# Kernel optimization log

Measured on AMD Instinct MI355X. Metric: run time of the kernel, lower is better.

Reference implementation:

```python
import jax, jax.numpy as jnp
import numpy as np
import math

INF = 1e12  # constant.INFINITY_NUMBER in the original repo


def setup_inputs() -> dict:
    key = jax.random.key(0)
    ks = jax.random.split(key, 12)
    B, S, W, D = 16, 512, 8, 768
    M, Wm = 2, 64
    U, Wu = 32, 16
    V = 32000
    words = jax.random.randint(ks[0], (B, S, W), 0, V)
    masks = jax.random.randint(ks[1], (B, S, W), 0, 2).astype(bool)
    main = jax.random.randint(ks[2], (B, M, Wm), 0, V)
    main_mask = jax.random.randint(ks[3], (B, M, Wm), 0, 2).astype(bool)
    user = jax.random.randint(ks[4], (B, U, Wu), 0, V)
    user_mask = jax.random.randint(ks[5], (B, U, Wu), 0, 2).astype(bool)
    # sparse-ish dependency adjacency
    adj = (jax.random.uniform(ks[6], (B, S, S)) < 0.05).astype(jnp.float32)
    emb_weight = jax.random.normal(ks[7], (V, D), jnp.float32) * 0.02
    K_w = jax.random.normal(ks[8], (D, D), jnp.float32) * (1.0 / math.sqrt(D))
    K_b = jnp.zeros((D,), jnp.float32)
    Q_w = jax.random.normal(ks[9], (D, D), jnp.float32) * (1.0 / math.sqrt(D))
    Q_b = jnp.zeros((D,), jnp.float32)
    return {"words": words, "masks": masks, "main": main, "main_mask": main_mask,
            "user": user, "user_mask": user_mask, "adj": adj,
            "emb_weight": emb_weight, "K_w": K_w, "K_b": K_b, "Q_w": Q_w, "Q_b": Q_b}


def _masked_max(embs, mask, axis):
    # masked_fill(mask, -INF) -> max(axis) ; caller fixes residual -INF rows
    return jnp.max(jnp.where(mask[..., None], -INF, embs), axis=axis)


def reference(words, masks, main, main_mask, user, user_mask, adj,
              emb_weight, K_w, K_b, Q_w, Q_b):
    D = emb_weight.shape[1]

    word_embs = emb_weight[words]   # [B,S,W,D]
    main_embs = emb_weight[main]    # [B,M,Wm,D]
    user_embs = emb_weight[user]    # [B,U,Wu,D]

    # node mask from adjacency: True where node has no in/out edges
    mask = ((adj.sum(axis=2) + adj.sum(axis=1)) == 0)[:, :, None]  # [B,S,1]

    # main: masked max-pool over word pieces, zero fully-masked rows
    main_e = _masked_max(main_embs, main_mask, axis=2)             # [B,M,D]
    main_e = jnp.where(main_e == -INF, 0.0, main_e)

    # user: masked max-pool over word pieces then over users
    user_e = _masked_max(user_embs, user_mask, axis=2)             # [B,U,D]
    user_e = jnp.max(user_e, axis=1)                               # [B,D]
    user_e = jnp.where(user_e == -INF, 0.0, user_e)

    # token embeddings: masked max-pool over word pieces (no -INF fix in original)
    g = _masked_max(word_embs, masks, axis=2)                      # [B,S,D]

    # single-head attention: softmax(K g (Q g)^T / sqrt(D)) @ g
    key_ = g @ K_w.T + K_b                                         # [B,S,D]
    query = g @ Q_w.T + Q_b                                        # [B,S,D]
    scores = jnp.einsum('bsd,btd->bst', key_, query) / math.sqrt(D)
    dense_graph = jax.nn.softmax(scores, axis=2)                   # [B,S,S]
    gcn_out = jnp.einsum('bst,btd->bsd', dense_graph, g)           # [B,S,D]

    adj_sm = jax.nn.softmax(adj, axis=2)

    return (gcn_out, mask, dense_graph, adj_sm,
            jnp.squeeze(main_e), jnp.squeeze(user_e))
```

## Files before the change

### kernel.cpp

```cpp
#include <hip/hip_runtime.h>
#include <hip/hip_bf16.h>
#include <math.h>

static constexpr int Bn = 16, Sn = 512, Wn = 8, Dn = 768;
static constexpr int Mn_ = 2, WMn = 64;
static constexpr int Un = 32, WUn = 16;

#define INF_VAL 1e12f
#define INV_SQRT_D 0.03608439182435161f

static constexpr size_t OFF_GCN   = 0;
static constexpr size_t OFF_MASK  = 6291456;
static constexpr size_t OFF_DENSE = 6299648;
static constexpr size_t OFF_ADJ   = 10493952;
static constexpr size_t OFF_MAIN  = 14688256;
static constexpr size_t OFF_USER  = 14712832;

static constexpr size_t WSB_GBF     = 0;
static constexpr size_t WSB_GT      = 12582912;
static constexpr size_t WSB_DENSEBF = 25165824;
static constexpr size_t WSB_HBF     = 33554432;
static constexpr size_t WSB_KWT     = 46137344;
static constexpr size_t WSB_QWT     = 47316992;
static constexpr size_t WSB_MT      = 48496640;
static constexpr size_t WSB_PARTU   = 49676288;
static constexpr size_t WSB_PARTM   = 51249152;
static constexpr size_t WSB_KBAR    = 51642368;
static constexpr size_t WSB_QBAR    = 51648512;
static constexpr size_t WSB_U       = 51654656;
static constexpr size_t WSB_V       = 51660800;
static constexpr size_t WSB_VA      = 51666944;
static constexpr size_t WSB_VB      = 51673088;
static constexpr size_t WSB_CONSTS  = 51679232;
static constexpr size_t WSB_QS      = 51679296;
static constexpr size_t WSB_KQ      = 51712064;
static constexpr size_t WSB_GA      = 51744832;
static constexpr size_t WSB_GB      = 51777600;
static constexpr size_t WSB_COLSUM  = 51810368;
static constexpr size_t WSB_FLAGS   = 51843136;
static constexpr size_t WSB_ROWSUM  = 51875904;
static constexpr size_t WSB_UVU     = 51908672;
static constexpr size_t WSB_UVV     = 51957824;
static constexpr size_t WSB_UVA     = 52006976;
static constexpr size_t WSB_UVB     = 52056128;

typedef __attribute__((ext_vector_type(8))) short short8;
typedef __attribute__((ext_vector_type(4))) float f32x4;

static __device__ __forceinline__ ushort f2bf(float f) {
    union { float f; unsigned u; } v; v.f = f;
    unsigned u = v.u;
    unsigned r = (u + 0x7FFFu + ((u >> 16) & 1u)) >> 16;
    return (ushort)r;
}

static __device__ __forceinline__ void gload16(const void* g, void* lds) {
    __builtin_amdgcn_global_load_lds(
        (const __attribute__((address_space(1))) void*)g,
        (__attribute__((address_space(3))) void*)lds, 16, 0, 0);
}

static __device__ __forceinline__ void fmax4(float4& a, const float4& x) {
    a.x = fmaxf(a.x, x.x); a.y = fmaxf(a.y, x.y);
    a.z = fmaxf(a.z, x.z); a.w = fmaxf(a.w, x.w);
}

__global__ __launch_bounds__(256)
void fold1(const float* __restrict__ K_w, const float* __restrict__ K_b,
           const float* __restrict__ Q_w, const float* __restrict__ Q_b,
           double* __restrict__ kbar, double* __restrict__ qbar,
           ushort* __restrict__ KwbT, ushort* __restrict__ QwbT,
           float* __restrict__ colsum) {
    int blk = blockIdx.x, t = threadIdx.x;
    if (blk < 192) {
        int wv = t >> 6, lane = t & 63;
        int r = blk * 4 + wv;
        double sk = 0.0, sq = 0.0;
        for (int d = lane; d < Dn; d += 64) {
            sk += (double)K_w[(size_t)r * Dn + d];
            sq += (double)Q_w[(size_t)r * Dn + d];
        }
        #pragma unroll
        for (int off = 32; off > 0; off >>= 1) {
            sk += __shfl_down(sk, off, 64);
            sq += __shfl_down(sq, off, 64);
        }
        if (lane == 0) {
            kbar[r] = -1e12 * sk + (double)K_b[r];
            qbar[r] = -1e12 * sq + (double)Q_b[r];
        }
    } else if (blk < 1344) {
        int tt = blk - 192;
        const float* src = (tt < 576) ? K_w : Q_w;
        ushort* dst = (tt < 576) ? KwbT : QwbT;
        int t6 = (tt < 576) ? tt : tt - 576;
        int e0 = (t6 % 24) * 32, i0 = (t6 / 24) * 32;
        __shared__ ushort tile[32][33];
        int tx = t & 31, ty = t >> 5;
        #pragma unroll
        for (int i2 = 0; i2 < 4; ++i2)
            tile[ty + i2 * 8][tx] = f2bf(src[(size_t)(e0 + ty + i2 * 8) * Dn + i0 + tx]);
        __syncthreads();
        #pragma unroll
        for (int i2 = 0; i2 < 4; ++i2)
            dst[(size_t)(i0 + ty + i2 * 8) * Dn + e0 + tx] = tile[tx][ty + i2 * 8];
    } else {
        for (int i = t; i < Bn * Sn; i += 256) colsum[i] = 0.f;
    }
}

__global__ __launch_bounds__(512)
void adjsm_uv_kernel(const float* __restrict__ adj, float* __restrict__ adjsm,
                     float* __restrict__ colsum, float* __restrict__ rowsum,
                     const float* __restrict__ K_w, const float* __restrict__ Q_w,
                     const float* __restrict__ K_b, const float* __restrict__ Q_b,
                     const double* __restrict__ kbar, const double* __restrict__ qbar,
                     double* __restrict__ uvu, double* __restrict__ uvv,
                     double* __restrict__ uva, double* __restrict__ uvb) {
    int blk = blockIdx.x;
    int t = threadIdx.x;
    if (blk >= 512) {
        int id = (blk - 512) * 512 + t;
        int c = id / 768;
        int j = id - c * 768;
        int e0 = c * 96;
        double su = 0.0, sv = 0.0, sa = 0.0, sb = 0.0;
        for (int e = e0; e < e0 + 96; ++e) {
            double kw = (double)K_w[(size_t)e * Dn + j];
            double qw = (double)Q_w[(size_t)e * Dn + j];
            su += kw * qbar[e];
            sv += qw * kbar[e];
            sa += kw * (double)Q_b[e];
            sb += qw * (double)K_b[e];
        }
        uvu[(size_t)c * Dn + j] = su;
        uvv[(size_t)c * Dn + j] = sv;
        uva[(size_t)c * Dn + j] = sa;
        uvb[(size_t)c * Dn + j] = sb;
        return;
    }
    int b = blk >> 5, rc = blk & 31;
    const float* base = adj + ((size_t)b * Sn + rc * 16) * Sn;
    float* obase = adjsm + ((size_t)b * Sn + rc * 16) * Sn;
    const float EM1 = 0.36787944117144233f;
    const float EP1 = 2.718281828459045f;
    __shared__ float red[8];
    float colacc = 0.f;
    for (int r = 0; r < 16; ++r) {
        float a = base[(size_t)r * Sn + t];
        colacc += a;
        float s = a;
        #pragma unroll
        for (int off = 32; off > 0; off >>= 1) s += __shfl_down(s, off, 64);
        if ((t & 63) == 0) red[t >> 6] = s;
        __syncthreads();
        float n1 = red[0] + red[1] + red[2] + red[3]
                 + red[4] + red[5] + red[6] + red[7];
        float e1, e0;
        if (n1 > 0.f) { e1 = 1.f; e0 = EM1; } else { e1 = EP1; e0 = 1.f; }
        float denom = n1 * e1 + (512.f - n1) * e0;
        float inv = 1.f / denom;
        obase[(size_t)r * Sn + t] = (a == 1.f ? e1 : e0) * inv;
        if (t == 0) rowsum[(size_t)b * Sn + rc * 16 + r] = n1;
        __syncthreads();
    }
    atomicAdd(&colsum[(size_t)b * Sn + t], colacc);
}

__global__ __launch_bounds__(64)
void uvred_consts(const double* __restrict__ uvu, const double* __restrict__ uvv,
                  const double* __restrict__ uva, const double* __restrict__ uvb,
                  const double* __restrict__ kbar, const double* __restrict__ qbar,
                  const float* __restrict__ K_b, const float* __restrict__ Q_b,
                  double* __restrict__ u, double* __restrict__ v,
                  double* __restrict__ va, double* __restrict__ vb,
                  double* __restrict__ consts) {
    int blk = blockIdx.x;
    int l = threadIdx.x;
    if (blk < 12) {
        int j = blk * 64 + l;
        double su = 0.0, sv = 0.0, sa = 0.0, sb = 0.0;
        #pragma unroll
        for (int c = 0; c < 8; ++c) {
            su += uvu[(size_t)c * Dn + j];
            sv += uvv[(size_t)c * Dn + j];
            sa += uva[(size_t)c * Dn + j];
            sb += uvb[(size_t)c * Dn + j];
        }
        u[j] = su; v[j] = sv; va[j] = sa; vb[j] = sb;
    } else {
        double c0 = 0.0, c1 = 0.0, c2 = 0.0, c3 = 0.0;
        for (int e = l; e < Dn; e += 64) {
            c0 += kbar[e] * (double)Q_b[e];
            c1 += kbar[e] * qbar[e];
            c2 += qbar[e] * (double)K_b[e];
            c3 += (double)K_b[e] * (double)Q_b[e];
        }
        #pragma unroll
        for (int off = 32; off > 0; off >>= 1) {
            c0 += __shfl_down(c0, off, 64);
            c1 += __shfl_down(c1, off, 64);
            c2 += __shfl_down(c2, off, 64);
            c3 += __shfl_down(c3, off, 64);
        }
        if (l == 0) { consts[0] = c0; consts[1] = c1; consts[2] = c2; consts[3] = c3; }
    }
}

__global__ __launch_bounds__(192)
void pool_g_s1(const int* __restrict__ words, const int* __restrict__ masks,
               const int* __restrict__ main_idx, const int* __restrict__ mmask,
               const int* __restrict__ user_idx, const int* __restrict__ umask,
               const float* __restrict__ emb,
               const double* __restrict__ u, const double* __restrict__ v,
               const double* __restrict__ va, const double* __restrict__ vb,
               const double* __restrict__ consts,
               ushort* __restrict__ gbf, float* __restrict__ qs,
               float* __restrict__ kq, float* __restrict__ ga,
               float* __restrict__ gb, int* __restrict__ flags,
               float* __restrict__ partM, float* __restrict__ partU) {
    int blk = blockIdx.x;
    int t = threadIdx.x;
    if (blk >= Bn * Sn) {
        int s1 = blk - Bn * Sn;
        const int *irow, *mrow;
        float* dst;
        if (s1 < 128) {
            int bm = s1 >> 2, ch = s1 & 3;
            irow = main_idx + (size_t)bm * WMn + ch * 16;
            mrow = mmask + (size_t)bm * WMn + ch * 16;
            dst = partM + (size_t)s1 * Dn;
        } else {
            int bu = s1 - 128;
            irow = user_idx + (size_t)bu * WUn;
            mrow = umask + (size_t)bu * WUn;
            dst = partU + (size_t)bu * Dn;
        }
        float4 acc = make_float4(-INF_VAL, -INF_VAL, -INF_VAL, -INF_VAL);
        #pragma unroll
        for (int w = 0; w < 16; ++w) {
            if (mrow[w] != 0) continue;
            float4 x = ((const float4*)(emb + (size_t)irow[w] * Dn))[t];
            fmax4(acc, x);
        }
        ((float4*)dst)[t] = acc;
        return;
    }
    int bs = blk;
    const int* wrow = words + (size_t)bs * Wn;
    const int* mrow = masks + (size_t)bs * Wn;
    float4 acc = make_float4(-INF_VAL, -INF_VAL, -INF_VAL, -INF_VAL);
    int nm = 0;
    #pragma unroll
    for (int w = 0; w < Wn; ++w) {
        int mk = mrow[w];
        nm += (mk != 0);
        if (mk != 0) continue;
        float4 x = ((const float4*)(emb + (size_t)wrow[w] * Dn))[t];
        fmax4(acc, x);
    }
    ushort4 o;
    o.x = f2bf(acc.x); o.y = f2bf(acc.y); o.z = f2bf(acc.z); o.w = f2bf(acc.w);
    ((ushort4*)(gbf + (size_t)bs * Dn))[t] = o;
    int j = t * 4;
    double dv = v[j] * (double)acc.x + v[j+1] * (double)acc.y
              + v[j+2] * (double)acc.z + v[j+3] * (double)acc.w;
    double du = u[j] * (double)acc.x + u[j+1] * (double)acc.y
              + u[j+2] * (double)acc.z + u[j+3] * (double)acc.w;
    double da = va[j] * (double)acc.x + va[j+1] * (double)acc.y
              + va[j+2] * (double)acc.z + va[j+3] * (double)acc.w;
    double db = vb[j] * (double)acc.x + vb[j+1] * (double)acc.y
              + vb[j+2] * (double)acc.z + vb[j+3] * (double)acc.w;
    #pragma unroll
    for (int off = 32; off > 0; off >>= 1) {
        dv += __shfl_down(dv, off, 64);
        du += __shfl_down(du, off, 64);
        da += __shfl_down(da, off, 64);
        db += __shfl_down(db, off, 64);
    }
    __shared__ double rr[12];
    if ((t & 63) == 0) {
        rr[t >> 6] = dv; rr[3 + (t >> 6)] = du;
        rr[6 + (t >> 6)] = da; rr[9 + (t >> 6)] = db;
    }
    __syncthreads();
    if (t == 0) {
        qs[bs] = (float)(rr[0] + rr[1] + rr[2] + consts[0]);
        kq[bs] = (float)(rr[3] + rr[4] + rr[5] + consts[2]);
        ga[bs] = (float)(rr[6] + rr[7] + rr[8]);
        gb[bs] = (float)(rr[9] + rr[10] + rr[11]);
        flags[bs] = (nm == Wn) ? 1 : 0;
    }
}

__global__ __launch_bounds__(256)
void mid_kernel(const ushort* __restrict__ gbf, ushort* __restrict__ gT,
                const float* __restrict__ partM, const float* __restrict__ partU,
                float* __restrict__ outM, float* __restrict__ outU,
                const float* __restrict__ rowsum, const float* __restrict__ colsum,
                float* __restrict__ maskout) {
    int blk = blockIdx.x;
    int t = threadIdx.x;
    if (blk < 6144) {
        __shared__ ushort tile[32][33];
        int b = blk / 384;
        int rem = blk - b * 384;
        int d0 = (rem % 24) * 32, s0 = (rem / 24) * 32;
        int tx = t & 31, ty = t >> 5;
        #pragma unroll
        for (int i = 0; i < 4; ++i)
            tile[ty + i * 8][tx] = gbf[((size_t)(b * Sn + s0 + ty + i * 8)) * Dn + d0 + tx];
        __syncthreads();
        #pragma unroll
        for (int i = 0; i < 4; ++i)
            gT[((size_t)(b * Dn + d0 + ty + i * 8)) * Sn + s0 + tx] = tile[tx][ty + i * 8];
        return;
    }
    if (blk >= 6192) {
        int i = (blk - 6192) * 256 + t;
        if (i < Bn * Sn)
            maskout[i] = ((rowsum[i] + colsum[i]) == 0.f) ? 1.f : 0.f;
        return;
    }
    if (t >= 192) return;
    float4 acc = make_float4(-INF_VAL, -INF_VAL, -INF_VAL, -INF_VAL);
    float* dst;
    if (blk < 6176) {
        int bm = blk - 6144;
        #pragma unroll
        for (int c = 0; c < 4; ++c) {
            float4 x = ((const float4*)(partM + (size_t)(bm * 4 + c) * Dn))[t];
            fmax4(acc, x);
        }
        dst = outM + (size_t)bm * Dn;
    } else {
        int b = blk - 6176;
        for (int u2 = 0; u2 < Un; ++u2) {
            float4 x = ((const float4*)(partU + (size_t)(b * Un + u2) * Dn))[t];
            fmax4(acc, x);
        }
        dst = outU + (size_t)b * Dn;
    }
    if (acc.x == -INF_VAL) acc.x = 0.f;
    if (acc.y == -INF_VAL) acc.y = 0.f;
    if (acc.z == -INF_VAL) acc.z = 0.f;
    if (acc.w == -INF_VAL) acc.w = 0.f;
    ((float4*)dst)[t] = acc;
}

template<int OUT_BF16>
__global__ __launch_bounds__(256)
void gemm_mfma(const ushort* __restrict__ A, const ushort* __restrict__ B,
               void* __restrict__ Cout,
               int Km, int lda, int ldb, int ldc,
               long long sA, long long sB, long long sC) {
    __shared__ ushort As[128 * 128];
    __shared__ ushort Bs[64 * 128];
    const ushort* Ab = A + (size_t)blockIdx.z * sA;
    const ushort* Bb = B + (size_t)blockIdx.z * sB;
    int i0 = blockIdx.y * 128, j0 = blockIdx.x * 64;
    int tid = threadIdx.x;
    int lane = tid & 63, wv = tid >> 6;
    int wr = wv >> 1, wc = wv & 1;
    int ln15 = lane & 15, lkg = lane >> 4;
    int r4 = lane >> 4;
    int c16 = lane & 15;

    f32x4 acc[4][2] = {};

    for (int k0 = 0; k0 < Km; k0 += 128) {
        #pragma unroll
        for (int it = 0; it < 8; ++it) {
            int r = it * 16 + wv * 4 + r4;
            int cc = c16 ^ (r & 15);
            ushort* dstA = As + (it * 4096 + wv * 1024) / 2;
            gload16(Ab + (size_t)(i0 + r) * lda + k0 + cc * 8, dstA);
        }
        #pragma unroll
        for (int it = 0; it < 4; ++it) {
            int r = it * 16 + wv * 4 + r4;
            int cc = c16 ^ (r & 15);
            ushort* dstB = Bs + (it * 4096 + wv * 1024) / 2;
            gload16(Bb + (size_t)(j0 + r) * ldb + k0 + cc * 8, dstB);
        }
        __syncthreads();
        #pragma unroll
        for (int kh = 0; kh < 4; ++kh) {
            short8 af[4], bfr[2];
            int kc = kh * 4 + lkg;
            #pragma unroll
            for (int f = 0; f < 4; ++f) {
                int ra = wr * 64 + f * 16 + ln15;
                af[f] = *(const short8*)((const char*)As + ra * 256 + ((kc ^ (ra & 15)) << 4));
            }
            #pragma unroll
            for (int f = 0; f < 2; ++f) {
                int rb = wc * 32 + f * 16 + ln15;
                bfr[f] = *(const short8*)((const char*)Bs + rb * 256 + ((kc ^ (rb & 15)) << 4));
            }
            #pragma unroll
            for (int fa = 0; fa < 4; ++fa)
                #pragma unroll
                for (int fb = 0; fb < 2; ++fb)
                    acc[fa][fb] = __builtin_amdgcn_mfma_f32_16x16x32_bf16(
                        af[fa], bfr[fb], acc[fa][fb], 0, 0, 0);
        }
        __syncthreads();
    }

    #pragma unroll
    for (int fa = 0; fa < 4; ++fa) {
        #pragma unroll
        for (int fb = 0; fb < 2; ++fb) {
            int n = j0 + wc * 32 + fb * 16 + ln15;
            #pragma unroll
            for (int rr = 0; rr < 4; ++rr) {
                int m = i0 + wr * 64 + fa * 16 + lkg * 4 + rr;
                float val = acc[fa][fb][rr];
                if (OUT_BF16) {
                    ((ushort*)Cout)[(size_t)blockIdx.z * sC + (size_t)m * ldc + n] = f2bf(val);
                } else {
                    ((float*)Cout)[(size_t)blockIdx.z * sC + (size_t)m * ldc + n] = val;
                }
            }
        }
    }
}

__global__ __launch_bounds__(256)
void softmax_fix(float* __restrict__ dense, const int* __restrict__ flags,
                 const float* __restrict__ qs, const float* __restrict__ kq,
                 const float* __restrict__ ga, const float* __restrict__ gb,
                 const double* __restrict__ consts, ushort* __restrict__ densebf) {
    int bs = blockIdx.x;
    int b = bs >> 9;
    int t = threadIdx.x;
    float* row = dense + (size_t)bs * 512;
    int f0 = flags[(b << 9) + t];
    int f1 = flags[(b << 9) + t + 256];
    bool sm = flags[bs] != 0;
    float x0, x1;
    if (sm) {
        float c1i = (float)consts[1] * INV_SQRT_D;
        x0 = f0 ? c1i : qs[(b << 9) + t] * INV_SQRT_D;
        x1 = f1 ? c1i : qs[(b << 9) + t + 256] * INV_SQRT_D;
    } else {
        float kqi = kq[bs] * INV_SQRT_D;
        float corr = ga[bs] + (float)consts[3];
        x0 = f0 ? kqi : (row[t] + corr + gb[(b << 9) + t]) * INV_SQRT_D;
        x1 = f1 ? kqi : (row[t + 256] + corr + gb[(b << 9) + t + 256]) * INV_SQRT_D;
    }
    float m = fmaxf(x0, x1);
    #pragma unroll
    for (int off = 32; off > 0; off >>= 1) m = fmaxf(m, __shfl_down(m, off, 64));
    __shared__ float red[4];
    __shared__ float bmax, bsum;
    if ((t & 63) == 0) red[t >> 6] = m;
    __syncthreads();
    if (t == 0) bmax = fmaxf(fmaxf(red[0], red[1]), fmaxf(red[2], red[3]));
    __syncthreads();
    float mx = bmax;
    float e0 = expf(x0 - mx), e1 = expf(x1 - mx);
    float s = e0 + e1;
    #pragma unroll
    for (int off = 32; off > 0; off >>= 1) s += __shfl_down(s, off, 64);
    if ((t & 63) == 0) red[t >> 6] = s;
    __syncthreads();
    if (t == 0) bsum = red[0] + red[1] + red[2] + red[3];
    __syncthreads();
    float inv = 1.f / bsum;
    float p0 = e0 * inv, p1 = e1 * inv;
    row[t] = p0; row[t + 256] = p1;
    ushort* bro = densebf + (size_t)bs * 512;
    bro[t] = f2bf(p0); bro[t + 256] = f2bf(p1);
}

extern "C" void kernel_launch(void* const* d_in, const int* in_sizes, int n_in,
                              void* d_out, int out_size, void* d_ws, size_t ws_size,
                              hipStream_t stream) {
    const int*   words     = (const int*)d_in[0];
    const int*   masks     = (const int*)d_in[1];
    const int*   main_idx  = (const int*)d_in[2];
    const int*   main_mask = (const int*)d_in[3];
    const int*   user_idx  = (const int*)d_in[4];
    const int*   user_mask = (const int*)d_in[5];
    const float* adj       = (const float*)d_in[6];
    const float* emb       = (const float*)d_in[7];
    const float* K_w       = (const float*)d_in[8];
    const float* K_b       = (const float*)d_in[9];
    const float* Q_w       = (const float*)d_in[10];
    const float* Q_b       = (const float*)d_in[11];

    float* out = (float*)d_out;
    char*  ws8 = (char*)d_ws;

    ushort* gbf     = (ushort*)(ws8 + WSB_GBF);
    ushort* gT      = (ushort*)(ws8 + WSB_GT);
    ushort* densebf = (ushort*)(ws8 + WSB_DENSEBF);
    ushort* hbf     = (ushort*)(ws8 + WSB_HBF);
    ushort* KwbT    = (ushort*)(ws8 + WSB_KWT);
    ushort* QwbT    = (ushort*)(ws8 + WSB_QWT);
    ushort* Mt      = (ushort*)(ws8 + WSB_MT);
    float*  partU   = (float*)(ws8 + WSB_PARTU);
    float*  partM   = (float*)(ws8 + WSB_PARTM);
    double* kbar    = (double*)(ws8 + WSB_KBAR);
    double* qbar    = (double*)(ws8 + WSB_QBAR);
    double* u       = (double*)(ws8 + WSB_U);
    double* v       = (double*)(ws8 + WSB_V);
    double* va      = (double*)(ws8 + WSB_VA);
    double* vb      = (double*)(ws8 + WSB_VB);
    double* consts  = (double*)(ws8 + WSB_CONSTS);
    float*  qs      = (float*)(ws8 + WSB_QS);
    float*  kq      = (float*)(ws8 + WSB_KQ);
    float*  ga      = (float*)(ws8 + WSB_GA);
    float*  gb      = (float*)(ws8 + WSB_GB);
    float*  colsum  = (float*)(ws8 + WSB_COLSUM);
    int*    flags   = (int*)(ws8 + WSB_FLAGS);
    float*  rowsum  = (float*)(ws8 + WSB_ROWSUM);
    double* uvu     = (double*)(ws8 + WSB_UVU);
    double* uvv     = (double*)(ws8 + WSB_UVV);
    double* uva     = (double*)(ws8 + WSB_UVA);
    double* uvb     = (double*)(ws8 + WSB_UVB);

    float* dense = out + OFF_DENSE;

    fold1<<<1345, 256, 0, stream>>>(K_w, K_b, Q_w, Q_b, kbar, qbar, KwbT, QwbT, colsum);

    adjsm_uv_kernel<<<524, 512, 0, stream>>>(adj, out + OFF_ADJ, colsum, rowsum,
                                             K_w, Q_w, K_b, Q_b, kbar, qbar,
                                             uvu, uvv, uva, uvb);

    uvred_consts<<<13, 64, 0, stream>>>(uvu, uvv, uva, uvb, kbar, qbar, K_b, Q_b,
                                        u, v, va, vb, consts);

    gemm_mfma<1><<<dim3(12, 6, 1), 256, 0, stream>>>(
        QwbT, KwbT, Mt, Dn, Dn, Dn, Dn, 0, 0, 0);

    pool_g_s1<<<Bn * Sn + 640, 192, 0, stream>>>(
        words, masks, main_idx, main_mask, user_idx, user_mask, emb,
        u, v, va, vb, consts, gbf, qs, kq, ga, gb, flags, partM, partU);

    mid_kernel<<<6224, 256, 0, stream>>>(gbf, gT, partM, partU,
                                         out + OFF_MAIN, out + OFF_USER,
                                         rowsum, colsum, out + OFF_MASK);

    gemm_mfma<1><<<dim3(12, 64, 1), 256, 0, stream>>>(
        gbf, Mt, hbf, Dn, Dn, Dn, Dn, 0, 0, 0);

    gemm_mfma<0><<<dim3(8, 4, Bn), 256, 0, stream>>>(
        hbf, gbf, dense, Dn, Dn, Dn, Sn,
        (long long)Sn * Dn, (long long)Sn * Dn, (long long)Sn * Sn);

    softmax_fix<<<Bn * Sn, 256, 0, stream>>>(dense, flags, qs, kq, ga, gb, consts, densebf);

    gemm_mfma<0><<<dim3(12, 4, Bn), 256, 0, stream>>>(
        densebf, gT, out + OFF_GCN, Sn, Sn, Sn, Dn,
        (long long)Sn * Sn, (long long)Dn * Sn, (long long)Sn * Dn);
}
```

Measured before the change: 157.3 us.

## Fuse small GEMMs into neighbouring kernels and restructure adjacency softmax row sums

Moves the GEMM body into a device function so it can share a launch with the uv reduction/constants kernel and with the transpose/pool/mask kernel, removing two kernel launches. The adjacency softmax now stages 16 rows in shared memory and computes each row sum once per wave instead of doing a block-wide reduction with syncthreads per row. In exchange, the fused kernels reserve GEMM-sized shared memory for every block, including the many tiny transpose blocks, which can reduce occupancy.

```diff
diff --git a/kernel.cpp b/kernel.cpp
--- a/kernel.cpp
+++ b/kernel.cpp
@@ -144,41 +144,151 @@
     float* obase = adjsm + ((size_t)b * Sn + rc * 16) * Sn;
     const float EM1 = 0.36787944117144233f;
     const float EP1 = 2.718281828459045f;
-    __shared__ float red[8];
+    __shared__ float rows[16][512];
+    __shared__ float n1s[16];
+    #pragma unroll
+    for (int r = 0; r < 16; ++r) rows[r][t] = base[(size_t)r * Sn + t];
+    __syncthreads();
+    int wv = t >> 6, lane = t & 63;
+    #pragma unroll
+    for (int rr2 = 0; rr2 < 2; ++rr2) {
+        int r = wv * 2 + rr2;
+        float s = 0.f;
+        #pragma unroll
+        for (int c = 0; c < 8; ++c) s += rows[r][lane + c * 64];
+        #pragma unroll
+        for (int off = 32; off > 0; off >>= 1) s += __shfl_down(s, off, 64);
+        if (lane == 0) {
+            n1s[r] = s;
+            rowsum[(size_t)b * Sn + rc * 16 + r] = s;
+        }
+    }
+    __syncthreads();
     float colacc = 0.f;
+    #pragma unroll
     for (int r = 0; r < 16; ++r) {
-        float a = base[(size_t)r * Sn + t];
+        float a = rows[r][t];
         colacc += a;
-        float s = a;
-        #pragma unroll
-        for (int off = 32; off > 0; off >>= 1) s += __shfl_down(s, off, 64);
-        if ((t & 63) == 0) red[t >> 6] = s;
-        __syncthreads();
-        float n1 = red[0] + red[1] + red[2] + red[3]
-                 + red[4] + red[5] + red[6] + red[7];
+        float n1 = n1s[r];
         float e1, e0;
         if (n1 > 0.f) { e1 = 1.f; e0 = EM1; } else { e1 = EP1; e0 = 1.f; }
-        float denom = n1 * e1 + (512.f - n1) * e0;
-        float inv = 1.f / denom;
+        float inv = 1.f / (n1 * e1 + (512.f - n1) * e0);
         obase[(size_t)r * Sn + t] = (a == 1.f ? e1 : e0) * inv;
-        if (t == 0) rowsum[(size_t)b * Sn + rc * 16 + r] = n1;
+    }
+    atomicAdd(&colsum[(size_t)b * Sn + t], colacc);
+}
+
+template<int OUT_BF16>
+static __device__ __forceinline__
+void gemm_device(const ushort* __restrict__ A, const ushort* __restrict__ B,
+                 void* __restrict__ Cout, int bx, int by, int bz,
+                 int Km, int lda, int ldb, int ldc,
+                 long long sA, long long sB, long long sC,
+                 ushort* As, ushort* Bs) {
+    const ushort* Ab = A + (size_t)bz * sA;
+    const ushort* Bb = B + (size_t)bz * sB;
+    int i0 = by * 128, j0 = bx * 64;
+    int tid = threadIdx.x;
+    int lane = tid & 63, wv = tid >> 6;
+    int wr = wv >> 1, wc = wv & 1;
+    int ln15 = lane & 15, lkg = lane >> 4;
+    int r4 = lane >> 4;
+    int c16 = lane & 15;
+
+    f32x4 acc[4][2] = {};
+
+    for (int k0 = 0; k0 < Km; k0 += 128) {
+        #pragma unroll
+        for (int it = 0; it < 8; ++it) {
+            int r = it * 16 + wv * 4 + r4;
+            int cc = c16 ^ (r & 15);
+            ushort* dstA = As + (it * 4096 + wv * 1024) / 2;
+            gload16(Ab + (size_t)(i0 + r) * lda + k0 + cc * 8, dstA);
+        }
+        #pragma unroll
+        for (int it = 0; it < 4; ++it) {
+            int r = it * 16 + wv * 4 + r4;
+            int cc = c16 ^ (r & 15);
+            ushort* dstB = Bs + (it * 4096 + wv * 1024) / 2;
+            gload16(Bb + (size_t)(j0 + r) * ldb + k0 + cc * 8, dstB);
+        }
         __syncthreads();
-    }
-    atomicAdd(&colsum[(size_t)b * Sn + t], colacc);
-}
-
-__global__ __launch_bounds__(64)
-void uvred_consts(const double* __restrict__ uvu, const double* __restrict__ uvv,
-                  const double* __restrict__ uva, const double* __restrict__ uvb,
-                  const double* __restrict__ kbar, const double* __restrict__ qbar,
-                  const float* __restrict__ K_b, const float* __restrict__ Q_b,
-                  double* __restrict__ u, double* __restrict__ v,
-                  double* __restrict__ va, double* __restrict__ vb,
-                  double* __restrict__ consts) {
+        #pragma unroll
+        for (int kh = 0; kh < 4; ++kh) {
+            short8 af[4], bfr[2];
+            int kc = kh * 4 + lkg;
+            #pragma unroll
+            for (int f = 0; f < 4; ++f) {
+                int ra = wr * 64 + f * 16 + ln15;
+                af[f] = *(const short8*)((const char*)As + ra * 256 + ((kc ^ (ra & 15)) << 4));
+            }
+            #pragma unroll
+            for (int f = 0; f < 2; ++f) {
+                int rb = wc * 32 + f * 16 + ln15;
+                bfr[f] = *(const short8*)((const char*)Bs + rb * 256 + ((kc ^ (rb & 15)) << 4));
+            }
+            #pragma unroll
+            for (int fa = 0; fa < 4; ++fa)
+                #pragma unroll
+                for (int fb = 0; fb < 2; ++fb)
+                    acc[fa][fb] = __builtin_amdgcn_mfma_f32_16x16x32_bf16(
+                        af[fa], bfr[fb], acc[fa][fb], 0, 0, 0);
+        }
+        __syncthreads();
+    }
+
+    #pragma unroll
+    for (int fa = 0; fa < 4; ++fa) {
+        #pragma unroll
+        for (int fb = 0; fb < 2; ++fb) {
+            int n = j0 + wc * 32 + fb * 16 + ln15;
+            #pragma unroll
+            for (int rr = 0; rr < 4; ++rr) {
+                int m = i0 + wr * 64 + fa * 16 + lkg * 4 + rr;
+                float val = acc[fa][fb][rr];
+                if (OUT_BF16) {
+                    ((ushort*)Cout)[(size_t)bz * sC + (size_t)m * ldc + n] = f2bf(val);
+                } else {
+                    ((float*)Cout)[(size_t)bz * sC + (size_t)m * ldc + n] = val;
+                }
+            }
+        }
+    }
+}
+
+template<int OUT_BF16>
+__global__ __launch_bounds__(256)
+void gemm_mfma(const ushort* __restrict__ A, const ushort* __restrict__ B,
+               void* __restrict__ Cout,
+               int Km, int lda, int ldb, int ldc,
+               long long sA, long long sB, long long sC) {
+    __shared__ ushort As[128 * 128];
+    __shared__ ushort Bs[64 * 128];
+    gemm_device<OUT_BF16>(A, B, Cout, blockIdx.x, blockIdx.y, blockIdx.z,
+                          Km, lda, ldb, ldc, sA, sB, sC, As, Bs);
+}
+
+__global__ __launch_bounds__(256)
+void uvmt_kernel(const ushort* __restrict__ QwbT, const ushort* __restrict__ KwbT,
+                 ushort* __restrict__ Mt,
+                 const double* __restrict__ uvu, const double* __restrict__ uvv,
+                 const double* __restrict__ uva, const double* __restrict__ uvb,
+                 const double* __restrict__ kbar, const double* __restrict__ qbar,
+                 const float* __restrict__ K_b, const float* __restrict__ Q_b,
+                 double* __restrict__ u, double* __restrict__ v,
+                 double* __restrict__ va, double* __restrict__ vb,
+                 double* __restrict__ consts) {
+    __shared__ ushort As[128 * 128];
+    __shared__ ushort Bs[64 * 128];
     int blk = blockIdx.x;
-    int l = threadIdx.x;
-    if (blk < 12) {
-        int j = blk * 64 + l;
+    int t = threadIdx.x;
+    if (blk < 72) {
+        gemm_device<1>(QwbT, KwbT, Mt, blk % 12, blk / 12, 0,
+                       Dn, Dn, Dn, Dn, 0, 0, 0, As, Bs);
+        return;
+    }
+    if (blk < 75) {
+        int j = (blk - 72) * 256 + t;
         double su = 0.0, sv = 0.0, sa = 0.0, sb = 0.0;
         #pragma unroll
         for (int c = 0; c < 8; ++c) {
@@ -188,23 +298,25 @@
             sb += uvb[(size_t)c * Dn + j];
         }
         u[j] = su; v[j] = sv; va[j] = sa; vb[j] = sb;
-    } else {
-        double c0 = 0.0, c1 = 0.0, c2 = 0.0, c3 = 0.0;
-        for (int e = l; e < Dn; e += 64) {
-            c0 += kbar[e] * (double)Q_b[e];
-            c1 += kbar[e] * qbar[e];
-            c2 += qbar[e] * (double)K_b[e];
-            c3 += (double)K_b[e] * (double)Q_b[e];
-        }
-        #pragma unroll
-        for (int off = 32; off > 0; off >>= 1) {
-            c0 += __shfl_down(c0, off, 64);
-            c1 += __shfl_down(c1, off, 64);
-            c2 += __shfl_down(c2, off, 64);
-            c3 += __shfl_down(c3, off, 64);
-        }
-        if (l == 0) { consts[0] = c0; consts[1] = c1; consts[2] = c2; consts[3] = c3; }
-    }
+        return;
+    }
+    if (t >= 64) return;
+    int l = t;
+    double c0 = 0.0, c1 = 0.0, c2 = 0.0, c3 = 0.0;
+    for (int e = l; e < Dn; e += 64) {
+        c0 += kbar[e] * (double)Q_b[e];
+        c1 += kbar[e] * qbar[e];
+        c2 += qbar[e] * (double)K_b[e];
+        c3 += (double)K_b[e] * (double)Q_b[e];
+    }
+    #pragma unroll
+    for (int off = 32; off > 0; off >>= 1) {
+        c0 += __shfl_down(c0, off, 64);
+        c1 += __shfl_down(c1, off, 64);
+        c2 += __shfl_down(c2, off, 64);
+        c3 += __shfl_down(c3, off, 64);
+    }
+    if (l == 0) { consts[0] = c0; consts[1] = c1; consts[2] = c2; consts[3] = c3; }
 }
 
 __global__ __launch_bounds__(192)
@@ -294,17 +406,26 @@
 }
 
 __global__ __launch_bounds__(256)
-void mid_kernel(const ushort* __restrict__ gbf, ushort* __restrict__ gT,
-                const float* __restrict__ partM, const float* __restrict__ partU,
-                float* __restrict__ outM, float* __restrict__ outU,
-                const float* __restrict__ rowsum, const float* __restrict__ colsum,
-                float* __restrict__ maskout) {
+void midh_kernel(const ushort* __restrict__ gbf, const ushort* __restrict__ Mt,
+                 ushort* __restrict__ hbf, ushort* __restrict__ gT,
+                 const float* __restrict__ partM, const float* __restrict__ partU,
+                 float* __restrict__ outM, float* __restrict__ outU,
+                 const float* __restrict__ rowsum, const float* __restrict__ colsum,
+                 float* __restrict__ maskout) {
+    __shared__ ushort As[128 * 128];
+    __shared__ ushort Bs[64 * 128];
     int blk = blockIdx.x;
     int t = threadIdx.x;
-    if (blk < 6144) {
-        __shared__ ushort tile[32][33];
-        int b = blk / 384;
-        int rem = blk - b * 384;
+    if (blk < 768) {
+        gemm_device<1>(gbf, Mt, hbf, blk % 12, blk / 12, 0,
+                       Dn, Dn, Dn, Dn, 0, 0, 0, As, Bs);
+        return;
+    }
+    if (blk < 6912) {
+        int bb = blk - 768;
+        ushort (*tile)[33] = (ushort(*)[33])As;
+        int b = bb / 384;
+        int rem = bb - b * 384;
         int d0 = (rem % 24) * 32, s0 = (rem / 24) * 32;
         int tx = t & 31, ty = t >> 5;
         #pragma unroll
@@ -316,8 +437,8 @@
             gT[((size_t)(b * Dn + d0 + ty + i * 8)) * Sn + s0 + tx] = tile[tx][ty + i * 8];
         return;
     }
-    if (blk >= 6192) {
-        int i = (blk - 6192) * 256 + t;
+    if (blk >= 6960) {
+        int i = (blk - 6960) * 256 + t;
         if (i < Bn * Sn)
             maskout[i] = ((rowsum[i] + colsum[i]) == 0.f) ? 1.f : 0.f;
         return;
@@ -325,8 +446,8 @@
     if (t >= 192) return;
     float4 acc = make_float4(-INF_VAL, -INF_VAL, -INF_VAL, -INF_VAL);
     float* dst;
-    if (blk < 6176) {
-        int bm = blk - 6144;
+    if (blk < 6944) {
+        int bm = blk - 6912;
         #pragma unroll
         for (int c = 0; c < 4; ++c) {
             float4 x = ((const float4*)(partM + (size_t)(bm * 4 + c) * Dn))[t];
@@ -334,7 +455,7 @@
         }
         dst = outM + (size_t)bm * Dn;
     } else {
-        int b = blk - 6176;
+        int b = blk - 6944;
         for (int u2 = 0; u2 < Un; ++u2) {
             float4 x = ((const float4*)(partU + (size_t)(b * Un + u2) * Dn))[t];
             fmax4(acc, x);
@@ -346,85 +467,6 @@
     if (acc.z == -INF_VAL) acc.z = 0.f;
     if (acc.w == -INF_VAL) acc.w = 0.f;
     ((float4*)dst)[t] = acc;
-}
-
-template<int OUT_BF16>
-__global__ __launch_bounds__(256)
-void gemm_mfma(const ushort* __restrict__ A, const ushort* __restrict__ B,
-               void* __restrict__ Cout,
-               int Km, int lda, int ldb, int ldc,
-               long long sA, long long sB, long long sC) {
-    __shared__ ushort As[128 * 128];
-    __shared__ ushort Bs[64 * 128];
-    const ushort* Ab = A + (size_t)blockIdx.z * sA;
-    const ushort* Bb = B + (size_t)blockIdx.z * sB;
-    int i0 = blockIdx.y * 128, j0 = blockIdx.x * 64;
-    int tid = threadIdx.x;
-    int lane = tid & 63, wv = tid >> 6;
-    int wr = wv >> 1, wc = wv & 1;
-    int ln15 = lane & 15, lkg = lane >> 4;
-    int r4 = lane >> 4;
-    int c16 = lane & 15;
-
-    f32x4 acc[4][2] = {};
-
-    for (int k0 = 0; k0 < Km; k0 += 128) {
-        #pragma unroll
-        for (int it = 0; it < 8; ++it) {
-            int r = it * 16 + wv * 4 + r4;
-            int cc = c16 ^ (r & 15);
-            ushort* dstA = As + (it * 4096 + wv * 1024) / 2;
-            gload16(Ab + (size_t)(i0 + r) * lda + k0 + cc * 8, dstA);
-        }
-        #pragma unroll
-        for (int it = 0; it < 4; ++it) {
-            int r = it * 16 + wv * 4 + r4;
-            int cc = c16 ^ (r & 15);
-            ushort* dstB = Bs + (it * 4096 + wv * 1024) / 2;
-            gload16(Bb + (size_t)(j0 + r) * ldb + k0 + cc * 8, dstB);
-        }
-        __syncthreads();
-        #pragma unroll
-        for (int kh = 0; kh < 4; ++kh) {
-            short8 af[4], bfr[2];
-            int kc = kh * 4 + lkg;
-            #pragma unroll
-            for (int f = 0; f < 4; ++f) {
-                int ra = wr * 64 + f * 16 + ln15;
-                af[f] = *(const short8*)((const char*)As + ra * 256 + ((kc ^ (ra & 15)) << 4));
-            }
-            #pragma unroll
-            for (int f = 0; f < 2; ++f) {
-                int rb = wc * 32 + f * 16 + ln15;
-                bfr[f] = *(const short8*)((const char*)Bs + rb * 256 + ((kc ^ (rb & 15)) << 4));
-            }
-            #pragma unroll
-            for (int fa = 0; fa < 4; ++fa)
-                #pragma unroll
-                for (int fb = 0; fb < 2; ++fb)
-                    acc[fa][fb] = __builtin_amdgcn_mfma_f32_16x16x32_bf16(
-                        af[fa], bfr[fb], acc[fa][fb], 0, 0, 0);
-        }
-        __syncthreads();
-    }
-
-    #pragma unroll
-    for (int fa = 0; fa < 4; ++fa) {
-        #pragma unroll
-        for (int fb = 0; fb < 2; ++fb) {
-            int n = j0 + wc * 32 + fb * 16 + ln15;
-            #pragma unroll
-            for (int rr = 0; rr < 4; ++rr) {
-                int m = i0 + wr * 64 + fa * 16 + lkg * 4 + rr;
-                float val = acc[fa][fb][rr];
-                if (OUT_BF16) {
-                    ((ushort*)Cout)[(size_t)blockIdx.z * sC + (size_t)m * ldc + n] = f2bf(val);
-                } else {
-                    ((float*)Cout)[(size_t)blockIdx.z * sC + (size_t)m * ldc + n] = val;
-                }
-            }
-        }
-    }
 }
 
 __global__ __launch_bounds__(256)
@@ -530,22 +572,16 @@
                                              K_w, Q_w, K_b, Q_b, kbar, qbar,
                                              uvu, uvv, uva, uvb);
 
-    uvred_consts<<<13, 64, 0, stream>>>(uvu, uvv, uva, uvb, kbar, qbar, K_b, Q_b,
-                                        u, v, va, vb, consts);
-
-    gemm_mfma<1><<<dim3(12, 6, 1), 256, 0, stream>>>(
-        QwbT, KwbT, Mt, Dn, Dn, Dn, Dn, 0, 0, 0);
+    uvmt_kernel<<<76, 256, 0, stream>>>(QwbT, KwbT, Mt, uvu, uvv, uva, uvb,
+                                        kbar, qbar, K_b, Q_b, u, v, va, vb, consts);
 
     pool_g_s1<<<Bn * Sn + 640, 192, 0, stream>>>(
         words, masks, main_idx, main_mask, user_idx, user_mask, emb,
         u, v, va, vb, consts, gbf, qs, kq, ga, gb, flags, partM, partU);
 
-    mid_kernel<<<6224, 256, 0, stream>>>(gbf, gT, partM, partU,
-                                         out + OFF_MAIN, out + OFF_USER,
-                                         rowsum, colsum, out + OFF_MASK);
-
-    gemm_mfma<1><<<dim3(12, 64, 1), 256, 0, stream>>>(
-        gbf, Mt, hbf, Dn, Dn, Dn, Dn, 0, 0, 0);
+    midh_kernel<<<6992, 256, 0, stream>>>(gbf, Mt, hbf, gT, partM, partU,
+                                          out + OFF_MAIN, out + OFF_USER,
+                                          rowsum, colsum, out + OFF_MASK);
 
     gemm_mfma<0><<<dim3(8, 4, Bn), 256, 0, stream>>>(
         hbf, gbf, dense, Dn, Dn, Dn, Sn,
```

After: 150.5 us. 1.05x faster.
